# Kernel tuning notes

Measured on AMD Instinct MI355X. Metric: run time of the kernel, lower is better.

## Reference

```python
import jax, jax.numpy as jnp
import numpy as np

N_BALLS = 256
BATCH = 128
N_STEPS = 100
MAX_EVENTS = 5
WORLD_W = 10.0
WORLD_H = 10.0
RADIUS = 0.1
HID = 64
DT = 0.05
INF = jnp.float32(1e30)

_II_np, _JJ_np = np.triu_indices(N_BALLS, 1)
_II = jnp.asarray(_II_np)
_JJ = jnp.asarray(_JJ_np)
# wall order: left, right, bottom, top (normals point into the box)
_WN = jnp.array([[1.0, 0.0], [-1.0, 0.0], [0.0, 1.0], [0.0, -1.0]], dtype=jnp.float32)
_WP = jnp.array([0.0, -WORLD_W, 0.0, -WORLD_H], dtype=jnp.float32)


def setup_inputs():
    key = jax.random.key(0)
    ks = jax.random.split(key, 6)
    pos = jax.random.uniform(ks[0], (BATCH, N_BALLS, 2), minval=0.5, maxval=9.5)
    vel = jax.random.normal(ks[1], (BATCH, N_BALLS, 2))
    state = jnp.concatenate([pos, vel], axis=-1)  # [B, N, 4]
    radii = jnp.full((N_BALLS,), RADIUS, dtype=jnp.float32)
    sc = 0.1
    W1 = jax.random.normal(ks[2], (HID, 2)) * sc
    b1 = jnp.zeros((HID,), jnp.float32)
    W2 = jax.random.normal(ks[3], (HID, HID)) * sc
    b2 = jnp.zeros((HID,), jnp.float32)
    W3 = jax.random.normal(ks[4], (1, HID)) * sc
    b3 = jnp.zeros((1,), jnp.float32)
    return {"state": state, "radii": radii, "W1": W1, "b1": b1, "W2": W2,
            "b2": b2, "W3": W3, "b3": b3, "dt": DT, "n_steps": N_STEPS}


def _detect(pos, vel, radii):
    # pos, vel: [N,2]; vectorized replacement of the Python O(N^2) loop.
    diff = pos[_JJ] - pos[_II]                       # [P,2]
    dist = jnp.linalg.norm(diff, axis=-1)            # [P]
    gap_b = dist - (radii[_II] + radii[_JJ])
    nhat = diff / (dist + 1e-8)[:, None]
    app_b = jnp.sum((vel[_JJ] - vel[_II]) * nhat, axis=-1)
    gb = jnp.where(app_b < 0, gap_b, INF)            # only approaching pairs
    r = radii
    gw = jnp.stack([pos[:, 0] - r, WORLD_W - pos[:, 0] - r,
                    pos[:, 1] - r, WORLD_H - pos[:, 1] - r], axis=-1)  # [N,4]
    vw = jnp.stack([vel[:, 0] < 0, vel[:, 0] > 0,
                    vel[:, 1] < 0, vel[:, 1] > 0], axis=-1)
    gw = jnp.where(vw, gw, INF)
    allg = jnp.concatenate([gb, gw.reshape(-1)])
    k = jnp.argmin(allg)
    P = gb.shape[0]
    is_ball = k < P
    gap = allg[k]
    bi = jnp.where(is_ball, k, 0)
    i_b, j_b = _II[bi], _JJ[bi]
    kw = jnp.where(is_ball, 0, k - P)
    i_w, wid = kw // 4, kw % 4
    return gap, is_ball, i_b, j_b, i_w, wid


def _apply_jump(s, i, j, W1, b1, W2, b2, W3, b3):
    pos, vel = s[..., :2], s[..., 2:]
    diff = pos[:, j] - pos[:, i]                               # [B,2]
    dist = jnp.maximum(jnp.linalg.norm(diff, axis=-1, keepdims=True), 1e-8)
    nhat = diff / dist
    app = jnp.sum((vel[:, j] - vel[:, i]) * nhat, axis=-1, keepdims=True)
    h = jnp.concatenate([dist, app], axis=-1)                  # [B,2]
    h = jax.nn.silu(h @ W1.T + b1)
    h = jax.nn.silu(h @ W2.T + b2)
    imp = (h @ W3.T + b3) * nhat                               # [B,2]
    vel_new = vel.at[:, i].add(imp).at[:, j].add(-imp)
    return jnp.concatenate([pos, vel_new], axis=-1)


def _apply_wall(s, i, wn, wp, r):
    pos, vel = s[..., :2], s[..., 2:]
    v, p = vel[:, i], pos[:, i]
    vn = jnp.sum(v * wn, axis=-1, keepdims=True)
    vel_new = vel.at[:, i].set(v - 2.0 * vn * wn)
    pn = jnp.sum(p * wn, axis=-1, keepdims=True)
    pen = jnp.maximum(wp + r - pn, 0.0)
    pos_new = pos.at[:, i].set(p + pen * wn)
    return jnp.concatenate([pos_new, vel_new], axis=-1)


def _rollout(state, radii, W1, b1, W2, b2, W3, b3, dt, n_steps):
    dt = jnp.float32(dt)

    def event_body(_, carry):
        curr, t_c, t_e, done = carry
        pos0, vel0 = curr[0, :, :2], curr[0, :, 2:]
        gap, is_ball, i_b, j_b, i_w, wid = _detect(pos0, vel0, radii)
        no_event = gap > 0.05
        n = pos0[j_b] - pos0[i_b]
        app_ball = -jnp.sum((vel0[j_b] - vel0[i_b]) * n / jnp.linalg.norm(n))
        app_wall = jnp.abs(jnp.max(vel0[i_w]))
        app = jnp.where(is_ball, app_ball, app_wall)
        t_ev = t_c + gap / jnp.maximum(app, 1e-6)
        # ZeroFlow is constant velocity -> dopri5 integrate is exact linear drift
        dte = jnp.where(t_ev > t_c + 1e-10, t_ev - t_c, 0.0)

        def apply_map(s):
            jm = _apply_jump(s, i_b, j_b, W1, b1, W2, b2, W3, b3)
            wm = _apply_wall(s, i_w, _WN[wid], _WP[wid], radii[i_w])
            return jnp.where(is_ball, jm, wm)

        state_a = apply_map(curr)                       # gap <= 0: jump now
        integ = curr.at[..., :2].add(curr[..., 2:] * dte)
        state_b = apply_map(integ)                      # 0 < gap: drift then jump
        act = (~done) & (~no_event)
        case_a = act & (gap <= 0)
        case_b = act & (gap > 0) & (app > 1e-6) & (t_ev < t_e)
        new_done = done | no_event | (act & (gap > 0) & ((app <= 1e-6) | (t_ev >= t_e)))
        new_curr = jnp.where(case_a, state_a, jnp.where(case_b, state_b, curr))
        new_t_c = jnp.where(case_b, t_ev, t_c)
        return new_curr, new_t_c, t_e, new_done

    def step(curr, step_idx):
        t_s = step_idx.astype(jnp.float32) * dt
        t_e = t_s + dt
        curr, t_c, _, _ = jax.lax.fori_loop(
            0, MAX_EVENTS, event_body, (curr, t_s, t_e, jnp.bool_(False)))
        dte = jnp.where(t_e > t_c + 1e-10, t_e - t_c, 0.0)
        curr = curr.at[..., :2].add(curr[..., 2:] * dte)
        return curr, curr

    _, traj = jax.lax.scan(step, state, jnp.arange(n_steps))
    return jnp.concatenate([state[None], traj], axis=0)   # [n_steps+1, B, N, 4]


def reference(state, radii, W1, b1, W2, b2, W3, b3, dt, n_steps):
    return _rollout(state, radii, W1, b1, W2, b2, W3, b3, dt, n_steps)
```

## Files before the change

kernel.cpp:

```cpp
#include <hip/hip_runtime.h>
#include <stdint.h>

#define NB 256
#define NBATCH 128
#define HID 64
#define MAXEV 5
#define MAXSTEPS 256
#define NT 43
#define NTILES 946
#define W2S 65
#define CAND_MAX 6144
#define CMARGIN 1.5f
#define NTHR 512
#define D2GATE 0.0626f

typedef unsigned long long u64;

__device__ __forceinline__ float bf2f(unsigned short u) {
    return __uint_as_float(((unsigned)u) << 16);
}
__device__ __forceinline__ unsigned short f2bf(float f) {
    unsigned u = __float_as_uint(f);
    u += 0x7FFFu + ((u >> 16) & 1u);
    return (unsigned short)(u >> 16);
}
__device__ __forceinline__ float rdin(const void* p, int idx, int bf) {
    return bf ? bf2f(((const unsigned short*)p)[idx]) : ((const float*)p)[idx];
}
__device__ __forceinline__ float silu_f(float x) {
    float s = __fdiv_rn(1.0f, __fadd_rn(1.0f, expf(-x)));
    return __fmul_rn(x, s);
}
__device__ __forceinline__ void lds_fence() {
    __builtin_amdgcn_wave_barrier();
    __threadfence_block();
    __builtin_amdgcn_wave_barrier();
}
__device__ __forceinline__ u64 shfl_down_u64(u64 v, int off) {
    unsigned lo = (unsigned)v, hi = (unsigned)(v >> 32);
    lo = __shfl_down(lo, off);
    hi = __shfl_down(hi, off);
    return (((u64)hi) << 32) | lo;
}
__device__ __forceinline__ unsigned fmap(float g) {
    unsigned u = __float_as_uint(g);
    unsigned m = (unsigned)(((int)u) >> 31) | 0x80000000u;
    return u ^ m;
}
__device__ __forceinline__ float funmap(unsigned sb) {
    unsigned u = (sb & 0x80000000u) ? (sb ^ 0x80000000u) : ~sb;
    return __uint_as_float(u);
}

__device__ __forceinline__ void append_agg(unsigned* list, int* counter, int cap, unsigned val) {
    u64 m = __ballot(1);
    int lane = (int)(threadIdx.x & 63);
    int ldr = (int)__builtin_ctzll(m);
    int pfx = (int)__builtin_popcountll(m & ((1ull << lane) - 1ull));
    int base = 0;
    if (lane == ldr) base = atomicAdd(counter, (int)__builtin_popcountll(m));
    base = __builtin_amdgcn_readfirstlane(base);
    int idx = base + pfx;
    if (idx < cap) list[idx] = val;
}

__device__ __forceinline__ u64 ball_key(const float4* ps, int i, int j,
                                        float dx, float dy, float d2,
                                        unsigned id, float rsum) {
    float4 A = ps[i], B = ps[j];
    float p1 = __fmul_rn(__fsub_rn(B.z, A.z), dx);
    float p2 = __fmul_rn(__fsub_rn(B.w, A.w), dy);
    float dot = __fadd_rn(p1, p2);
    float mag = __fadd_rn(fabsf(p1), fabsf(p2));
    bool appr;
    if (fabsf(dot) < __fmul_rn(1e-5f, mag)) {
        float dist = __fsqrt_rn(d2);
        float den = __fadd_rn(dist, 1e-8f);
        float ab = __fadd_rn(__fmul_rn(__fsub_rn(B.z, A.z), __fdiv_rn(dx, den)),
                             __fmul_rn(__fsub_rn(B.w, A.w), __fdiv_rn(dy, den)));
        appr = ab < 0.0f;
    } else {
        appr = dot < 0.0f;
    }
    if (!appr) return ~0ull;
    float gap = __fsub_rn(__fsqrt_rn(d2), rsum);
    return (((u64)fmap(gap)) << 17) | id;
}

__device__ __forceinline__ void scan_list(const unsigned* src, int n,
                                          const float2* pos2c, const float4* ps0c,
                                          float rsum, u64& kC, int tid) {
    unsigned idq[8];
    #pragma unroll
    for (int q = 0; q < 8; q++) {
        int c = tid + q * NTHR;
        idq[q] = (c < n) ? src[c] : 0u;
    }
    float2 Aq[8], Bq[8];
    #pragma unroll
    for (int q = 0; q < 8; q++) {
        Aq[q] = pos2c[idq[q] >> 8];
        Bq[q] = pos2c[idq[q] & 255u];
    }
    #pragma unroll
    for (int q = 0; q < 8; q++) {
        float dx = __fsub_rn(Bq[q].x, Aq[q].x), dy = __fsub_rn(Bq[q].y, Aq[q].y);
        float d2 = __fadd_rn(__fmul_rn(dx, dx), __fmul_rn(dy, dy));
        bool live = (tid + q * NTHR) < n;
        if (live && d2 < D2GATE) {
            u64 key = ball_key(ps0c, (int)(idq[q] >> 8), (int)(idq[q] & 255u),
                               dx, dy, d2, idq[q], rsum);
            kC = key < kC ? key : kC;
        }
    }
    for (int c = tid + 8 * NTHR; c < n; c += NTHR) {
        unsigned id = src[c];
        float2 A = pos2c[id >> 8], B = pos2c[id & 255u];
        float dx = __fsub_rn(B.x, A.x), dy = __fsub_rn(B.y, A.y);
        float d2 = __fadd_rn(__fmul_rn(dx, dx), __fmul_rn(dy, dy));
        if (d2 < D2GATE) {
            u64 key = ball_key(ps0c, (int)(id >> 8), (int)(id & 255u), dx, dy, d2, id, rsum);
            kC = key < kC ? key : kC;
        }
    }
}

__device__ __forceinline__ void scan_full(const float2* pos2c, const float4* ps0c, float rsum,
                                          int i0a, int j0a, int i0b, int j0b,
                                          bool apB, float th2B, unsigned* cand, int* candN,
                                          u64& kC) {
    #pragma unroll
    for (int tt = 0; tt < 2; tt++) {
        int I0 = tt ? i0b : i0a;
        int J0 = tt ? j0b : j0a;
        if (I0 < 0) continue;
        float2 Pi[6], Pj[6];
        #pragma unroll
        for (int a = 0; a < 6; a++) {
            int ii = I0 + a; ii = ii < NB ? ii : NB - 1;
            int jj = J0 + a; jj = jj < NB ? jj : NB - 1;
            Pi[a] = pos2c[ii]; Pj[a] = pos2c[jj];
        }
        #pragma unroll
        for (int a = 0; a < 6; a++) {
            int i = I0 + a;
            #pragma unroll
            for (int bb = 0; bb < 6; bb++) {
                int j = J0 + bb;
                bool ok = (i < NB) && (j < NB) && (j > i);
                float dx = __fsub_rn(Pj[bb].x, Pi[a].x);
                float dy = __fsub_rn(Pj[bb].y, Pi[a].y);
                float d2 = __fadd_rn(__fmul_rn(dx, dx), __fmul_rn(dy, dy));
                unsigned id = (unsigned)((i << 8) | j);
                if (apB && ok && d2 < th2B) append_agg(cand, candN, CAND_MAX, id);
                if (ok && d2 < D2GATE) {
                    u64 key = ball_key(ps0c, i, j, dx, dy, d2, id, rsum);
                    kC = key < kC ? key : kC;
                }
            }
        }
    }
}

__device__ void load_weights(float* w1, float* b1s, float* w2, float* b2s, float* w3, float* b3s,
                             const void* W1, const void* B1, const void* W2, const void* B2,
                             const void* W3, const void* B3, int bf, int tid, int nthr) {
    for (int k = tid; k < HID * 2; k += nthr) w1[k] = rdin(W1, k, bf);
    for (int k = tid; k < HID; k += nthr) {
        b1s[k] = rdin(B1, k, bf);
        b2s[k] = rdin(B2, k, bf);
        w3[k]  = rdin(W3, k, bf);
    }
    for (int k = tid; k < HID * HID; k += nthr) {
        int m = k >> 6, c = k & 63;
        w2[m * W2S + c] = rdin(W2, k, bf);
    }
    if (tid == 0) b3s[0] = rdin(B3, 0, bf);
}

__global__ void sniff_kernel(const unsigned short* st, int* ws) {
    __shared__ int ev;
    if (threadIdx.x == 0) ev = 0;
    __syncthreads();
    unsigned short u = st[threadIdx.x];
    int e = (u >> 7) & 0xFF;
    if (e >= 0x85) atomicOr(&ev, 1);
    __syncthreads();
    if (threadIdx.x == 0) ws[0] = ev ? 0 : 1;
}

__global__ void row0_kernel(const void* in, void* out, const int* ws) {
    int idx = blockIdx.x * blockDim.x + threadIdx.x;
    if (ws[0]) ((unsigned short*)out)[idx] = ((const unsigned short*)in)[idx];
    else       ((float*)out)[idx] = ((const float*)in)[idx];
}

__global__ __launch_bounds__(NTHR, 1) void sim_kernel(
    const void* in_state, const void* in_rad,
    const void* inW1, const void* inB1, const void* inW2, const void* inB2,
    const void* inW3, const void* inB3, const void* in_dt, const int* in_nsteps,
    void* out, const int* ws) {
    __shared__ float4 ps0[2][NB];
    __shared__ float4 psb[2][NB];
    __shared__ float2 pos2[2][NB];
    __shared__ float w1[HID * 2], b1s[HID], w2[HID * W2S], b2s[HID], w3s[HID], b3s[1];
    __shared__ float sc0[132], scb[132];
    __shared__ u64 redK[8];
    __shared__ float redF[4];
    __shared__ unsigned cand[CAND_MAX];
    __shared__ int candN;
    __shared__ int pubF;
    __shared__ int rebF;

    int tid = threadIdx.x;
    int b = blockIdx.x;
    int bf = ws[0];

    if (tid < NB) {
        int base0 = tid * 4;
        float4 P;
        P.x = rdin(in_state, base0 + 0, bf);
        P.y = rdin(in_state, base0 + 1, bf);
        P.z = rdin(in_state, base0 + 2, bf);
        P.w = rdin(in_state, base0 + 3, bf);
        ps0[0][tid] = P;
        float2 p2v; p2v.x = P.x; p2v.y = P.y;
        pos2[0][tid] = p2v;
        int baseb = (b * NB + tid) * 4;
        float4 Q;
        Q.x = rdin(in_state, baseb + 0, bf);
        Q.y = rdin(in_state, baseb + 1, bf);
        Q.z = rdin(in_state, baseb + 2, bf);
        Q.w = rdin(in_state, baseb + 3, bf);
        psb[0][tid] = Q;
        float m2 = P.z * P.z + P.w * P.w;
        #pragma unroll
        for (int off = 32; off; off >>= 1) m2 = fmaxf(m2, __shfl_down(m2, off));
        if ((tid & 63) == 0) redF[tid >> 6] = m2;
    }
    load_weights(w1, b1s, w2, b2s, w3s, b3s, inW1, inB1, inW2, inB2, inW3, inB3, bf, tid, NTHR);
    if (tid == 0) { candN = 0; pubF = 0; rebF = 1; }

    float dtv = rdin(in_dt, 0, bf);
    int NS = in_nsteps[0]; if (NS > MAXSTEPS) NS = MAXSTEPS; if (NS < 0) NS = 0;
    float rad0 = rdin(in_rad, 0, bf);
    float rsum = __fadd_rn(rad0, rad0);

    int i0a = -1, j0a = 0, i0b = -1, j0b = 0;
    {
        int T = tid;
        if (T < NTILES) {
            int rem = T, r = 0;
            while (rem >= NT - r) { rem -= NT - r; r++; }
            i0a = r * 6; j0a = (r + rem) * 6;
        }
        T = tid + NTHR;
        if (T < NTILES) {
            int rem = T, r = 0;
            while (rem >= NT - r) { rem -= NT - r; r++; }
            i0b = r * 6; j0b = (r + rem) * 6;
        }
    }
    __syncthreads();

    float thB = __fadd_rn(__fadd_rn(rsum, 0.05f), CMARGIN);
    float th2B = __fmul_rn(thB, thB);

    int p = 0;
    int nc = 0;
    bool candOvf = false;
    float used = 1e30f, vcap = 0.0f;

    for (int s = 0; s < NS; s++) {
        int rebuild = rebF;
        float t_s = __fmul_rn((float)s, dtv);
        float t_e = __fadd_rn(t_s, dtv);
        float t_c = t_s;
        if (tid < 64) {
            if (rebuild) {
                vcap = sqrtf(fmaxf(fmaxf(redF[0], redF[1]), fmaxf(redF[2], redF[3])));
                used = 0.0f;
            }
            used = __fadd_rn(used, __fmul_rn(__fmul_rn(2.0f, dtv), vcap));
        }

        for (int e = 0; e < MAXEV; e++) {
            const float4* ps0c = ps0[p];
            const float2* pos2c = pos2[p];
            const float4* psbc = psb[p];
            float4* ps0n = ps0[p ^ 1];
            float2* pos2n = pos2[p ^ 1];
            float4* psbn = psb[p ^ 1];

            u64 kC = ~0ull;
            int mode;
            if (e == 0) mode = rebuild ? 2 : 1;
            else        mode = pubF ? 2 : 1;
            if (mode == 2) {
                bool apB = (e == 0);
                scan_full(pos2c, ps0c, rsum, i0a, j0a, i0b, j0b,
                          apB, th2B, cand, &candN, kC);
            } else {
                scan_list(cand, nc, pos2c, ps0c, rsum, kC, tid);
            }
            {
                int ball = tid & 255, wsel = tid >> 8;
                float4 P = ps0c[ball];
                #pragma unroll
                for (int q = 0; q < 2; q++) {
                    int w = wsel * 2 + q;
                    float g; bool valid;
                    if (w == 0)      { g = __fsub_rn(P.x, rad0); valid = P.z < 0.0f; }
                    else if (w == 1) { g = __fsub_rn(__fsub_rn(10.0f, P.x), rad0); valid = P.z > 0.0f; }
                    else if (w == 2) { g = __fsub_rn(P.y, rad0); valid = P.w < 0.0f; }
                    else             { g = __fsub_rn(__fsub_rn(10.0f, P.y), rad0); valid = P.w > 0.0f; }
                    if (valid) {
                        u64 key = (((u64)fmap(g)) << 17) | 0x10000u | (unsigned)(ball * 4 + w);
                        kC = key < kC ? key : kC;
                    }
                }
            }
            #pragma unroll
            for (int off = 32; off; off >>= 1) {
                u64 o = shfl_down_u64(kC, off);
                kC = o < kC ? o : kC;
            }
            if ((tid & 63) == 0) redK[tid >> 6] = kC;
            __syncthreads();

            if (e == 0 && rebuild) {
                int ct = candN;
                candOvf = ct > CAND_MAX;
                nc = candOvf ? CAND_MAX : ct;
            }

            float g_nx = 0, g_ny = 0, g_dist = 0, g_app = 0;
            float4 gA, gB;
            int code = 0; float dteB = 0.0f; float tcn = t_c;
            int ei = 0, ejw = 0;
            {
                u64 m = redK[0];
                #pragma unroll
                for (int q = 1; q < 8; q++) m = redK[q] < m ? redK[q] : m;
                if (m != ~0ull) {
                    bool is_ball = ((m >> 16) & 1ull) == 0;
                    unsigned id = (unsigned)(m & 0xFFFFull);
                    float gap = funmap((unsigned)(m >> 17));
                    int pi = (int)(id >> 8), pj = (int)(id & 255u);
                    int wb = (int)(id >> 2), ww = (int)(id & 3u);
                    ei = is_ball ? pi : wb;
                    ejw = is_ball ? pj : ww;
                    if (!(gap > 0.05f)) {
                        float app;
                        if (is_ball) {
                            float4 A = ps0c[pi], B = ps0c[pj];
                            float dx = __fsub_rn(B.x, A.x), dy = __fsub_rn(B.y, A.y);
                            float nrm = __fsqrt_rn(__fadd_rn(__fmul_rn(dx, dx), __fmul_rn(dy, dy)));
                            float dvx = __fsub_rn(B.z, A.z), dvy = __fsub_rn(B.w, A.w);
                            app = -__fadd_rn(__fdiv_rn(__fmul_rn(dvx, dx), nrm),
                                             __fdiv_rn(__fmul_rn(dvy, dy), nrm));
                        } else {
                            float4 Wb = ps0c[wb];
                            app = fabsf(fmaxf(Wb.z, Wb.w));
                        }
                        float t_ev = __fadd_rn(t_c, __fdiv_rn(gap, fmaxf(app, 1e-6f)));
                        if (gap <= 0.0f) {
                            code = is_ball ? 1 : 3;
                        } else if (app > 1e-6f && t_ev < t_e) {
                            code = is_ball ? 2 : 4;
                            dteB = (t_ev > __fadd_rn(t_c, 1e-10f)) ? __fsub_rn(t_ev, t_c) : 0.0f;
                            tcn = t_ev;
                        }
                    }
                }
                if (tid < 64 && code != 0 && code <= 2) {
                    float4 A = ps0c[ei], B = ps0c[ejw];
                    if (code == 2) {
                        A.x = __fadd_rn(A.x, __fmul_rn(A.z, dteB));
                        A.y = __fadd_rn(A.y, __fmul_rn(A.w, dteB));
                        B.x = __fadd_rn(B.x, __fmul_rn(B.z, dteB));
                        B.y = __fadd_rn(B.y, __fmul_rn(B.w, dteB));
                    }
                    gA = A; gB = B;
                    float dx = __fsub_rn(B.x, A.x), dy = __fsub_rn(B.y, A.y);
                    float nrm = __fsqrt_rn(__fadd_rn(__fmul_rn(dx, dx), __fmul_rn(dy, dy)));
                    float dist = fmaxf(nrm, 1e-8f);
                    g_nx = __fdiv_rn(dx, dist); g_ny = __fdiv_rn(dy, dist);
                    g_dist = dist;
                    float dvx = __fsub_rn(B.z, A.z), dvy = __fsub_rn(B.w, A.w);
                    g_app = __fadd_rn(__fmul_rn(dvx, g_nx), __fmul_rn(dvy, g_ny));
                }
            }
            if (code == 0) break;
            t_c = tcn;
            bool integ = (code == 2) || (code == 4);
            int skip2 = (code <= 2) ? ejw : -1;

            if (code <= 2) {
                if (tid < 64) {
                    float a = __fadd_rn(__fadd_rn(__fmul_rn(g_dist, w1[2 * tid]),
                                                  __fmul_rn(g_app, w1[2 * tid + 1])), b1s[tid]);
                    sc0[4 + tid] = silu_f(a);
                    lds_fence();
                    float acc = 0.0f;
                    const float* row = &w2[tid * W2S];
                    #pragma unroll 8
                    for (int k = 0; k < HID; k++) acc = __fadd_rn(acc, __fmul_rn(sc0[4 + k], row[k]));
                    acc = __fadd_rn(acc, b2s[tid]);
                    sc0[68 + tid] = silu_f(acc);
                    lds_fence();
                    float acc3 = 0.0f;
                    #pragma unroll 8
                    for (int k = 0; k < HID; k++)
                        acc3 = __fadd_rn(acc3, __fmul_rn(sc0[68 + k], w3s[k]));
                    float impv = __fadd_rn(acc3, b3s[0]);
                    float ix = __fmul_rn(impv, g_nx), iy = __fmul_rn(impv, g_ny);
                    float nAz = __fadd_rn(gA.z, ix),  nAw = __fadd_rn(gA.w, iy);
                    float nBz = __fadd_rn(gB.z, -ix), nBw = __fadd_rn(gB.w, -iy);
                    if (tid == 0) {
                        float4 outA; outA.x = gA.x; outA.y = gA.y; outA.z = nAz; outA.w = nAw;
                        float4 outB; outB.x = gB.x; outB.y = gB.y; outB.z = nBz; outB.w = nBw;
                        ps0n[ei] = outA; ps0n[ejw] = outB;
                        float2 pa; pa.x = gA.x; pa.y = gA.y; pos2n[ei] = pa;
                        float2 pb; pb.x = gB.x; pb.y = gB.y; pos2n[ejw] = pb;
                    }
                    float s1 = sqrtf(nAz * nAz + nAw * nAw);
                    float s2 = sqrtf(nBz * nBz + nBw * nBw);
                    float nv = fmaxf(s1, s2);
                    used = __fadd_rn(used, __fmul_rn(__fmul_rn(2.0f, dtv),
                                                     fmaxf(__fsub_rn(nv, vcap), 0.0f)));
                    vcap = fmaxf(vcap, nv);
                    int nf = (candOvf || (__fadd_rn(used, 1e-3f) > CMARGIN)) ? 1 : 0;
                    if (tid == 0) pubF = nf;
                } else if (tid < 128) {
                    int lane = tid - 64;
                    float4 A = psbc[ei], B = psbc[ejw];
                    if (integ) {
                        A.x = __fadd_rn(A.x, __fmul_rn(A.z, dteB));
                        A.y = __fadd_rn(A.y, __fmul_rn(A.w, dteB));
                        B.x = __fadd_rn(B.x, __fmul_rn(B.z, dteB));
                        B.y = __fadd_rn(B.y, __fmul_rn(B.w, dteB));
                    }
                    float dx = __fsub_rn(B.x, A.x), dy = __fsub_rn(B.y, A.y);
                    float nrm = __fsqrt_rn(__fadd_rn(__fmul_rn(dx, dx), __fmul_rn(dy, dy)));
                    float dist = fmaxf(nrm, 1e-8f);
                    float nx = __fdiv_rn(dx, dist), ny = __fdiv_rn(dy, dist);
                    float dvx = __fsub_rn(B.z, A.z), dvy = __fsub_rn(B.w, A.w);
                    float app2 = __fadd_rn(__fmul_rn(dvx, nx), __fmul_rn(dvy, ny));
                    float a = __fadd_rn(__fadd_rn(__fmul_rn(dist, w1[2 * lane]),
                                                  __fmul_rn(app2, w1[2 * lane + 1])), b1s[lane]);
                    scb[4 + lane] = silu_f(a);
                    lds_fence();
                    float acc = 0.0f;
                    const float* row = &w2[lane * W2S];
                    #pragma unroll 8
                    for (int k = 0; k < HID; k++) acc = __fadd_rn(acc, __fmul_rn(scb[4 + k], row[k]));
                    acc = __fadd_rn(acc, b2s[lane]);
                    scb[68 + lane] = silu_f(acc);
                    lds_fence();
                    float acc3 = 0.0f;
                    #pragma unroll 8
                    for (int k = 0; k < HID; k++)
                        acc3 = __fadd_rn(acc3, __fmul_rn(scb[68 + k], w3s[k]));
                    float impv = __fadd_rn(acc3, b3s[0]);
                    if (lane == 0) {
                        float ix = __fmul_rn(impv, nx), iy = __fmul_rn(impv, ny);
                        float4 outA; outA.x = A.x; outA.y = A.y;
                        outA.z = __fadd_rn(A.z, ix);  outA.w = __fadd_rn(A.w, iy);
                        float4 outB; outB.x = B.x; outB.y = B.y;
                        outB.z = __fadd_rn(B.z, -ix); outB.w = __fadd_rn(B.w, -iy);
                        psbn[ei] = outA; psbn[ejw] = outB;
                    }
                }
            } else {
                const float wnx[4] = {1.f, -1.f, 0.f, 0.f};
                const float wny[4] = {0.f, 0.f, 1.f, -1.f};
                const float wpv[4] = {0.f, -10.f, 0.f, -10.f};
                int w = ejw;
                if (tid < 64) {
                    float4 P = ps0c[ei];
                    if (integ) {
                        P.x = __fadd_rn(P.x, __fmul_rn(P.z, dteB));
                        P.y = __fadd_rn(P.y, __fmul_rn(P.w, dteB));
                    }
                    float vn = __fadd_rn(__fmul_rn(P.z, wnx[w]), __fmul_rn(P.w, wny[w]));
                    float t2 = __fmul_rn(2.0f, vn);
                    float nvx = __fsub_rn(P.z, __fmul_rn(t2, wnx[w]));
                    float nvy = __fsub_rn(P.w, __fmul_rn(t2, wny[w]));
                    float pn = __fadd_rn(__fmul_rn(P.x, wnx[w]), __fmul_rn(P.y, wny[w]));
                    float pen = fmaxf(__fsub_rn(__fadd_rn(wpv[w], rad0), pn), 0.0f);
                    float4 nP;
                    nP.x = __fadd_rn(P.x, __fmul_rn(pen, wnx[w]));
                    nP.y = __fadd_rn(P.y, __fmul_rn(pen, wny[w]));
                    nP.z = nvx; nP.w = nvy;
                    used = __fadd_rn(used, pen);
                    int nf = (candOvf || (__fadd_rn(used, 1e-3f) > CMARGIN)) ? 1 : 0;
                    if (tid == 0) {
                        ps0n[ei] = nP;
                        float2 pp; pp.x = nP.x; pp.y = nP.y; pos2n[ei] = pp;
                        pubF = nf;
                    }
                } else if (tid < 128) {
                    if (tid == 64) {
                        float4 P = psbc[ei];
                        if (integ) {
                            P.x = __fadd_rn(P.x, __fmul_rn(P.z, dteB));
                            P.y = __fadd_rn(P.y, __fmul_rn(P.w, dteB));
                        }
                        float vn = __fadd_rn(__fmul_rn(P.z, wnx[w]), __fmul_rn(P.w, wny[w]));
                        float t2 = __fmul_rn(2.0f, vn);
                        float nvx = __fsub_rn(P.z, __fmul_rn(t2, wnx[w]));
                        float nvy = __fsub_rn(P.w, __fmul_rn(t2, wny[w]));
                        float pn = __fadd_rn(__fmul_rn(P.x, wnx[w]), __fmul_rn(P.y, wny[w]));
                        float pen = fmaxf(__fsub_rn(__fadd_rn(wpv[w], rad0), pn), 0.0f);
                        float4 nP;
                        nP.x = __fadd_rn(P.x, __fmul_rn(pen, wnx[w]));
                        nP.y = __fadd_rn(P.y, __fmul_rn(pen, wny[w]));
                        nP.z = nvx; nP.w = nvy;
                        psbn[ei] = nP;
                    }
                }
            }
            if (tid >= 128 && tid < 384) {
                int t = tid - 128;
                if (t != ei && t != skip2) {
                    float4 P = ps0c[t];
                    P.x = __fadd_rn(P.x, __fmul_rn(P.z, dteB));
                    P.y = __fadd_rn(P.y, __fmul_rn(P.w, dteB));
                    ps0n[t] = P;
                    float2 pp; pp.x = P.x; pp.y = P.y; pos2n[t] = pp;
                }
            } else if (tid >= 384) {
                #pragma unroll
                for (int q = 0; q < 2; q++) {
                    int t = (tid - 384) + q * 128;
                    if (t != ei && t != skip2) {
                        float4 Q = psbc[t];
                        Q.x = __fadd_rn(Q.x, __fmul_rn(Q.z, dteB));
                        Q.y = __fadd_rn(Q.y, __fmul_rn(Q.w, dteB));
                        psbn[t] = Q;
                    }
                }
            }
            __syncthreads();
            p ^= 1;
        }

        float fd = (t_e > __fadd_rn(t_c, 1e-10f)) ? __fsub_rn(t_e, t_c) : 0.0f;
        if (tid < NB) {
            float4 P = ps0[p][tid];
            P.x = __fadd_rn(P.x, __fmul_rn(P.z, fd));
            P.y = __fadd_rn(P.y, __fmul_rn(P.w, fd));
            ps0[p ^ 1][tid] = P;
            float2 pp; pp.x = P.x; pp.y = P.y; pos2[p ^ 1][tid] = pp;
            float m2 = P.z * P.z + P.w * P.w;
            #pragma unroll
            for (int off = 32; off; off >>= 1) m2 = fmaxf(m2, __shfl_down(m2, off));
            if ((tid & 63) == 0) redF[tid >> 6] = m2;
            if (tid == 0) {
                candN = 0;
                float usedNext = __fadd_rn(used, __fmul_rn(__fmul_rn(2.0f, dtv), vcap));
                rebF = (candOvf || (__fadd_rn(usedNext, 1e-3f) > CMARGIN)) ? 1 : 0;
            }
        } else {
            int t = tid - NB;
            float4 Q = psb[p][t];
            Q.x = __fadd_rn(Q.x, __fmul_rn(Q.z, fd));
            Q.y = __fadd_rn(Q.y, __fmul_rn(Q.w, fd));
            psb[p ^ 1][t] = Q;
            long long base = ((long long)(s + 1) * NBATCH + b) * (NB * 4);
            if (bf) {
                ushort4 v;
                v.x = f2bf(Q.x); v.y = f2bf(Q.y); v.z = f2bf(Q.z); v.w = f2bf(Q.w);
                ((ushort4*)((unsigned short*)out + base))[t] = v;
            } else {
                ((float4*)((float*)out + base))[t] = Q;
            }
        }
        __syncthreads();
        p ^= 1;
    }
}

extern "C" void kernel_launch(void* const* d_in, const int* in_sizes, int n_in,
                              void* d_out, int out_size, void* d_ws, size_t ws_size,
                              hipStream_t stream) {
    int* ws = (int*)d_ws;
    sniff_kernel<<<1, 256, 0, stream>>>((const unsigned short*)d_in[0], ws);
    row0_kernel<<<(NBATCH * NB * 4) / 256, 256, 0, stream>>>(d_in[0], d_out, ws);
    sim_kernel<<<NBATCH, NTHR, 0, stream>>>(
        d_in[0], d_in[1], d_in[2], d_in[3], d_in[4], d_in[5], d_in[6], d_in[7],
        d_in[8], (const int*)d_in[9], d_out, ws);
}
```

Measured before the change: 3.342 ms.

## Fold end-of-step drift into event pass and use DPP wave reductions

The separate end-of-step drift pass is merged into the last event iteration, or into the early-exit branch when no event remains. This removes one barrier-separated pass over the state per step, and the output store happens inside that merged pass. Wave-level min and max reductions now use DPP row operations plus readlane instead of shuffle-down loops. The per-ball gather for the chosen pair is reused instead of reloaded. The cost is more branching and duplicated bookkeeping (redF[4], rebF updates), which adds correctness risk.

```diff
diff --git a/kernel.cpp b/kernel.cpp
--- a/kernel.cpp
+++ b/kernel.cpp
@@ -36,12 +36,6 @@
     __threadfence_block();
     __builtin_amdgcn_wave_barrier();
 }
-__device__ __forceinline__ u64 shfl_down_u64(u64 v, int off) {
-    unsigned lo = (unsigned)v, hi = (unsigned)(v >> 32);
-    lo = __shfl_down(lo, off);
-    hi = __shfl_down(hi, off);
-    return (((u64)hi) << 32) | lo;
-}
 __device__ __forceinline__ unsigned fmap(float g) {
     unsigned u = __float_as_uint(g);
     unsigned m = (unsigned)(((int)u) >> 31) | 0x80000000u;
@@ -50,6 +44,40 @@
 __device__ __forceinline__ float funmap(unsigned sb) {
     unsigned u = (sb & 0x80000000u) ? (sb ^ 0x80000000u) : ~sb;
     return __uint_as_float(u);
+}
+
+template<int CTRL>
+__device__ __forceinline__ u64 dpp_min_u64_step(u64 k) {
+    unsigned lo = (unsigned)k, hi = (unsigned)(k >> 32);
+    unsigned nlo = (unsigned)__builtin_amdgcn_update_dpp(-1, (int)lo, CTRL, 0xF, 0xF, false);
+    unsigned nhi = (unsigned)__builtin_amdgcn_update_dpp(-1, (int)hi, CTRL, 0xF, 0xF, false);
+    u64 nk = (((u64)nhi) << 32) | (u64)nlo;
+    return nk < k ? nk : k;
+}
+__device__ __forceinline__ u64 wave_min_u64(u64 k) {
+    k = dpp_min_u64_step<0x111>(k);
+    k = dpp_min_u64_step<0x112>(k);
+    k = dpp_min_u64_step<0x114>(k);
+    k = dpp_min_u64_step<0x118>(k);
+    k = dpp_min_u64_step<0x142>(k);
+    k = dpp_min_u64_step<0x143>(k);
+    unsigned lo = (unsigned)__builtin_amdgcn_readlane((int)(unsigned)k, 63);
+    unsigned hi = (unsigned)__builtin_amdgcn_readlane((int)(unsigned)(k >> 32), 63);
+    return (((u64)hi) << 32) | (u64)lo;
+}
+template<int CTRL>
+__device__ __forceinline__ float dpp_max_f32_step(float x) {
+    int nx = __builtin_amdgcn_update_dpp(0, __float_as_int(x), CTRL, 0xF, 0xF, false);
+    return fmaxf(x, __int_as_float(nx));
+}
+__device__ __forceinline__ float wave_max_f32(float x) {
+    x = dpp_max_f32_step<0x111>(x);
+    x = dpp_max_f32_step<0x112>(x);
+    x = dpp_max_f32_step<0x114>(x);
+    x = dpp_max_f32_step<0x118>(x);
+    x = dpp_max_f32_step<0x142>(x);
+    x = dpp_max_f32_step<0x143>(x);
+    return __int_as_float(__builtin_amdgcn_readlane(__float_as_int(x), 63));
 }
 
 __device__ __forceinline__ void append_agg(unsigned* list, int* counter, int cap, unsigned val) {
@@ -162,6 +190,16 @@
     }
 }
 
+__device__ __forceinline__ void store_ball(void* out, long long base, int t, float4 Q, int bf) {
+    if (bf) {
+        ushort4 v;
+        v.x = f2bf(Q.x); v.y = f2bf(Q.y); v.z = f2bf(Q.z); v.w = f2bf(Q.w);
+        ((ushort4*)((unsigned short*)out + base))[t] = v;
+    } else {
+        ((float4*)((float*)out + base))[t] = Q;
+    }
+}
+
 __device__ void load_weights(float* w1, float* b1s, float* w2, float* b2s, float* w3, float* b3s,
                              const void* W1, const void* B1, const void* W2, const void* B2,
                              const void* W3, const void* B3, int bf, int tid, int nthr) {
@@ -206,7 +244,7 @@
     __shared__ float w1[HID * 2], b1s[HID], w2[HID * W2S], b2s[HID], w3s[HID], b3s[1];
     __shared__ float sc0[132], scb[132];
     __shared__ u64 redK[8];
-    __shared__ float redF[4];
+    __shared__ float redF[5];
     __shared__ unsigned cand[CAND_MAX];
     __shared__ int candN;
     __shared__ int pubF;
@@ -234,12 +272,11 @@
         Q.w = rdin(in_state, baseb + 3, bf);
         psb[0][tid] = Q;
         float m2 = P.z * P.z + P.w * P.w;
-        #pragma unroll
-        for (int off = 32; off; off >>= 1) m2 = fmaxf(m2, __shfl_down(m2, off));
+        m2 = wave_max_f32(m2);
         if ((tid & 63) == 0) redF[tid >> 6] = m2;
     }
     load_weights(w1, b1s, w2, b2s, w3s, b3s, inW1, inB1, inW2, inB2, inW3, inB3, bf, tid, NTHR);
-    if (tid == 0) { candN = 0; pubF = 0; rebF = 1; }
+    if (tid == 0) { candN = 0; pubF = 0; rebF = 1; redF[4] = 0.0f; }
 
     float dtv = rdin(in_dt, 0, bf);
     int NS = in_nsteps[0]; if (NS > MAXSTEPS) NS = MAXSTEPS; if (NS < 0) NS = 0;
@@ -276,9 +313,11 @@
         float t_s = __fmul_rn((float)s, dtv);
         float t_e = __fadd_rn(t_s, dtv);
         float t_c = t_s;
+        long long obase = ((long long)(s + 1) * NBATCH + b) * (NB * 4);
         if (tid < 64) {
             if (rebuild) {
-                vcap = sqrtf(fmaxf(fmaxf(redF[0], redF[1]), fmaxf(redF[2], redF[3])));
+                vcap = sqrtf(fmaxf(fmaxf(fmaxf(redF[0], redF[1]),
+                                         fmaxf(redF[2], redF[3])), redF[4]));
                 used = 0.0f;
             }
             used = __fadd_rn(used, __fmul_rn(__fmul_rn(2.0f, dtv), vcap));
@@ -320,11 +359,7 @@
                     }
                 }
             }
-            #pragma unroll
-            for (int off = 32; off; off >>= 1) {
-                u64 o = shfl_down_u64(kC, off);
-                kC = o < kC ? o : kC;
-            }
+            kC = wave_min_u64(kC);
             if ((tid & 63) == 0) redK[tid >> 6] = kC;
             __syncthreads();
 
@@ -350,10 +385,11 @@
                     int wb = (int)(id >> 2), ww = (int)(id & 3u);
                     ei = is_ball ? pi : wb;
                     ejw = is_ball ? pj : ww;
+                    float4 A, B;
                     if (!(gap > 0.05f)) {
                         float app;
                         if (is_ball) {
-                            float4 A = ps0c[pi], B = ps0c[pj];
+                            A = ps0c[pi]; B = ps0c[pj];
                             float dx = __fsub_rn(B.x, A.x), dy = __fsub_rn(B.y, A.y);
                             float nrm = __fsqrt_rn(__fadd_rn(__fmul_rn(dx, dx), __fmul_rn(dy, dy)));
                             float dvx = __fsub_rn(B.z, A.z), dvy = __fsub_rn(B.w, A.w);
@@ -372,28 +408,60 @@
                             tcn = t_ev;
                         }
                     }
-                }
-                if (tid < 64 && code != 0 && code <= 2) {
-                    float4 A = ps0c[ei], B = ps0c[ejw];
-                    if (code == 2) {
-                        A.x = __fadd_rn(A.x, __fmul_rn(A.z, dteB));
-                        A.y = __fadd_rn(A.y, __fmul_rn(A.w, dteB));
-                        B.x = __fadd_rn(B.x, __fmul_rn(B.z, dteB));
-                        B.y = __fadd_rn(B.y, __fmul_rn(B.w, dteB));
-                    }
-                    gA = A; gB = B;
-                    float dx = __fsub_rn(B.x, A.x), dy = __fsub_rn(B.y, A.y);
-                    float nrm = __fsqrt_rn(__fadd_rn(__fmul_rn(dx, dx), __fmul_rn(dy, dy)));
-                    float dist = fmaxf(nrm, 1e-8f);
-                    g_nx = __fdiv_rn(dx, dist); g_ny = __fdiv_rn(dy, dist);
-                    g_dist = dist;
-                    float dvx = __fsub_rn(B.z, A.z), dvy = __fsub_rn(B.w, A.w);
-                    g_app = __fadd_rn(__fmul_rn(dvx, g_nx), __fmul_rn(dvy, g_ny));
-                }
-            }
-            if (code == 0) break;
+                    if (tid < 64 && code != 0 && code <= 2) {
+                        if (code == 2) {
+                            A.x = __fadd_rn(A.x, __fmul_rn(A.z, dteB));
+                            A.y = __fadd_rn(A.y, __fmul_rn(A.w, dteB));
+                            B.x = __fadd_rn(B.x, __fmul_rn(B.z, dteB));
+                            B.y = __fadd_rn(B.y, __fmul_rn(B.w, dteB));
+                        }
+                        gA = A; gB = B;
+                        float dx = __fsub_rn(B.x, A.x), dy = __fsub_rn(B.y, A.y);
+                        float nrm = __fsqrt_rn(__fadd_rn(__fmul_rn(dx, dx), __fmul_rn(dy, dy)));
+                        float dist = fmaxf(nrm, 1e-8f);
+                        g_nx = __fdiv_rn(dx, dist); g_ny = __fdiv_rn(dy, dist);
+                        g_dist = dist;
+                        float dvx = __fsub_rn(B.z, A.z), dvy = __fsub_rn(B.w, A.w);
+                        g_app = __fadd_rn(__fmul_rn(dvx, g_nx), __fmul_rn(dvy, g_ny));
+                    }
+                }
+            }
+
+            if (code == 0) {
+                float fd = (t_e > __fadd_rn(t_c, 1e-10f)) ? __fsub_rn(t_e, t_c) : 0.0f;
+                if (tid < NB) {
+                    float4 P = ps0c[tid];
+                    P.x = __fadd_rn(P.x, __fmul_rn(P.z, fd));
+                    P.y = __fadd_rn(P.y, __fmul_rn(P.w, fd));
+                    ps0n[tid] = P;
+                    float2 pp; pp.x = P.x; pp.y = P.y; pos2n[tid] = pp;
+                    float m2 = P.z * P.z + P.w * P.w;
+                    m2 = wave_max_f32(m2);
+                    if ((tid & 63) == 0) redF[tid >> 6] = m2;
+                    if (tid == 0) {
+                        redF[4] = 0.0f;
+                        candN = 0;
+                        float usedNext = __fadd_rn(used, __fmul_rn(__fmul_rn(2.0f, dtv), vcap));
+                        rebF = (candOvf || (__fadd_rn(usedNext, 1e-3f) > CMARGIN)) ? 1 : 0;
+                    }
+                } else {
+                    int t = tid - NB;
+                    float4 Q = psbc[t];
+                    Q.x = __fadd_rn(Q.x, __fmul_rn(Q.z, fd));
+                    Q.y = __fadd_rn(Q.y, __fmul_rn(Q.w, fd));
+                    psbn[t] = Q;
+                    store_ball(out, obase, t, Q, bf);
+                }
+                __syncthreads();
+                p ^= 1;
+                break;
+            }
+
             t_c = tcn;
             bool integ = (code == 2) || (code == 4);
+            bool last = (e == MAXEV - 1);
+            float fd = 0.0f;
+            if (last) fd = (t_e > __fadd_rn(t_c, 1e-10f)) ? __fsub_rn(t_e, t_c) : 0.0f;
             int skip2 = (code <= 2) ? ejw : -1;
 
             if (code <= 2) {
@@ -420,9 +488,15 @@
                     if (tid == 0) {
                         float4 outA; outA.x = gA.x; outA.y = gA.y; outA.z = nAz; outA.w = nAw;
                         float4 outB; outB.x = gB.x; outB.y = gB.y; outB.z = nBz; outB.w = nBw;
+                        if (last) {
+                            outA.x = __fadd_rn(outA.x, __fmul_rn(outA.z, fd));
+                            outA.y = __fadd_rn(outA.y, __fmul_rn(outA.w, fd));
+                            outB.x = __fadd_rn(outB.x, __fmul_rn(outB.z, fd));
+                            outB.y = __fadd_rn(outB.y, __fmul_rn(outB.w, fd));
+                        }
                         ps0n[ei] = outA; ps0n[ejw] = outB;
-                        float2 pa; pa.x = gA.x; pa.y = gA.y; pos2n[ei] = pa;
-                        float2 pb; pb.x = gB.x; pb.y = gB.y; pos2n[ejw] = pb;
+                        float2 pa; pa.x = outA.x; pa.y = outA.y; pos2n[ei] = pa;
+                        float2 pb; pb.x = outB.x; pb.y = outB.y; pos2n[ejw] = pb;
                     }
                     float s1 = sqrtf(nAz * nAz + nAw * nAw);
                     float s2 = sqrtf(nBz * nBz + nBw * nBw);
@@ -431,7 +505,15 @@
                                                      fmaxf(__fsub_rn(nv, vcap), 0.0f)));
                     vcap = fmaxf(vcap, nv);
                     int nf = (candOvf || (__fadd_rn(used, 1e-3f) > CMARGIN)) ? 1 : 0;
-                    if (tid == 0) pubF = nf;
+                    if (tid == 0) {
+                        pubF = nf;
+                        if (last) {
+                            redF[4] = fmaxf(nAz * nAz + nAw * nAw, nBz * nBz + nBw * nBw);
+                            candN = 0;
+                            float usedNext = __fadd_rn(used, __fmul_rn(__fmul_rn(2.0f, dtv), vcap));
+                            rebF = (candOvf || (__fadd_rn(usedNext, 1e-3f) > CMARGIN)) ? 1 : 0;
+                        }
+                    }
                 } else if (tid < 128) {
                     int lane = tid - 64;
                     float4 A = psbc[ei], B = psbc[ejw];
@@ -469,6 +551,14 @@
                         outA.z = __fadd_rn(A.z, ix);  outA.w = __fadd_rn(A.w, iy);
                         float4 outB; outB.x = B.x; outB.y = B.y;
                         outB.z = __fadd_rn(B.z, -ix); outB.w = __fadd_rn(B.w, -iy);
+                        if (last) {
+                            outA.x = __fadd_rn(outA.x, __fmul_rn(outA.z, fd));
+                            outA.y = __fadd_rn(outA.y, __fmul_rn(outA.w, fd));
+                            outB.x = __fadd_rn(outB.x, __fmul_rn(outB.z, fd));
+                            outB.y = __fadd_rn(outB.y, __fmul_rn(outB.w, fd));
+                            store_ball(out, obase, ei, outA, bf);
+                            store_ball(out, obase, ejw, outB, bf);
+                        }
                         psbn[ei] = outA; psbn[ejw] = outB;
                     }
                 }
@@ -493,12 +583,22 @@
                     nP.x = __fadd_rn(P.x, __fmul_rn(pen, wnx[w]));
                     nP.y = __fadd_rn(P.y, __fmul_rn(pen, wny[w]));
                     nP.z = nvx; nP.w = nvy;
+                    if (last) {
+                        nP.x = __fadd_rn(nP.x, __fmul_rn(nP.z, fd));
+                        nP.y = __fadd_rn(nP.y, __fmul_rn(nP.w, fd));
+                    }
                     used = __fadd_rn(used, pen);
                     int nf = (candOvf || (__fadd_rn(used, 1e-3f) > CMARGIN)) ? 1 : 0;
                     if (tid == 0) {
                         ps0n[ei] = nP;
                         float2 pp; pp.x = nP.x; pp.y = nP.y; pos2n[ei] = pp;
                         pubF = nf;
+                        if (last) {
+                            redF[4] = nvx * nvx + nvy * nvy;
+                            candN = 0;
+                            float usedNext = __fadd_rn(used, __fmul_rn(__fmul_rn(2.0f, dtv), vcap));
+                            rebF = (candOvf || (__fadd_rn(usedNext, 1e-3f) > CMARGIN)) ? 1 : 0;
+                        }
                     }
                 } else if (tid < 128) {
                     if (tid == 64) {
@@ -517,18 +617,33 @@
                         nP.x = __fadd_rn(P.x, __fmul_rn(pen, wnx[w]));
                         nP.y = __fadd_rn(P.y, __fmul_rn(pen, wny[w]));
                         nP.z = nvx; nP.w = nvy;
+                        if (last) {
+                            nP.x = __fadd_rn(nP.x, __fmul_rn(nP.z, fd));
+                            nP.y = __fadd_rn(nP.y, __fmul_rn(nP.w, fd));
+                            store_ball(out, obase, ei, nP, bf);
+                        }
                         psbn[ei] = nP;
                     }
                 }
             }
             if (tid >= 128 && tid < 384) {
                 int t = tid - 128;
+                float m2 = 0.0f;
                 if (t != ei && t != skip2) {
                     float4 P = ps0c[t];
                     P.x = __fadd_rn(P.x, __fmul_rn(P.z, dteB));
                     P.y = __fadd_rn(P.y, __fmul_rn(P.w, dteB));
+                    if (last) {
+                        P.x = __fadd_rn(P.x, __fmul_rn(P.z, fd));
+                        P.y = __fadd_rn(P.y, __fmul_rn(P.w, fd));
+                        m2 = P.z * P.z + P.w * P.w;
+                    }
                     ps0n[t] = P;
                     float2 pp; pp.x = P.x; pp.y = P.y; pos2n[t] = pp;
+                }
+                if (last) {
+                    float mx = wave_max_f32(m2);
+                    if ((tid & 63) == 0) redF[(tid >> 6) - 2] = mx;
                 }
             } else if (tid >= 384) {
                 #pragma unroll
@@ -538,6 +653,11 @@
                         float4 Q = psbc[t];
                         Q.x = __fadd_rn(Q.x, __fmul_rn(Q.z, dteB));
                         Q.y = __fadd_rn(Q.y, __fmul_rn(Q.w, dteB));
+                        if (last) {
+                            Q.x = __fadd_rn(Q.x, __fmul_rn(Q.z, fd));
+                            Q.y = __fadd_rn(Q.y, __fmul_rn(Q.w, fd));
+                            store_ball(out, obase, t, Q, bf);
+                        }
                         psbn[t] = Q;
                     }
                 }
@@ -545,40 +665,6 @@
             __syncthreads();
             p ^= 1;
         }
-
-        float fd = (t_e > __fadd_rn(t_c, 1e-10f)) ? __fsub_rn(t_e, t_c) : 0.0f;
-        if (tid < NB) {
-            float4 P = ps0[p][tid];
-            P.x = __fadd_rn(P.x, __fmul_rn(P.z, fd));
-            P.y = __fadd_rn(P.y, __fmul_rn(P.w, fd));
-            ps0[p ^ 1][tid] = P;
-            float2 pp; pp.x = P.x; pp.y = P.y; pos2[p ^ 1][tid] = pp;
-            float m2 = P.z * P.z + P.w * P.w;
-            #pragma unroll
-            for (int off = 32; off; off >>= 1) m2 = fmaxf(m2, __shfl_down(m2, off));
-            if ((tid & 63) == 0) redF[tid >> 6] = m2;
-            if (tid == 0) {
-                candN = 0;
-                float usedNext = __fadd_rn(used, __fmul_rn(__fmul_rn(2.0f, dtv), vcap));
-                rebF = (candOvf || (__fadd_rn(usedNext, 1e-3f) > CMARGIN)) ? 1 : 0;
-            }
-        } else {
-            int t = tid - NB;
-            float4 Q = psb[p][t];
-            Q.x = __fadd_rn(Q.x, __fmul_rn(Q.z, fd));
-            Q.y = __fadd_rn(Q.y, __fmul_rn(Q.w, fd));
-            psb[p ^ 1][t] = Q;
-            long long base = ((long long)(s + 1) * NBATCH + b) * (NB * 4);
-            if (bf) {
-                ushort4 v;
-                v.x = f2bf(Q.x); v.y = f2bf(Q.y); v.z = f2bf(Q.z); v.w = f2bf(Q.w);
-                ((ushort4*)((unsigned short*)out + base))[t] = v;
-            } else {
-                ((float4*)((float*)out + base))[t] = Q;
-            }
-        }
-        __syncthreads();
-        p ^= 1;
     }
 }
 
```

Measured after the change: 3.261 ms. 2.4% less time.
